# Kernel tuning notes

Hardware: AMD Instinct MI355X
Metric: run time of the kernel (lower is better)

Reference implementation:

```python
import jax, jax.numpy as jnp
import numpy as np

CLASS_NUM = 6
N = 8388608


def setup_inputs() -> dict:
    key = jax.random.key(0)
    k1, k2, k3 = jax.random.split(key, 3)
    inputs = jax.random.normal(k1, (N, CLASS_NUM), dtype=jnp.float32)
    targets = jax.random.randint(k2, (N, 1), 0, CLASS_NUM, dtype=jnp.int32)
    # learned parameter: torch.rand(class_num) -> uniform [0,1)
    class_weight = jax.random.uniform(k3, (CLASS_NUM,), dtype=jnp.float32)
    return {"inputs": inputs, "targets": targets, "class_weight": class_weight}


def reference(inputs, targets, class_weight):
    # weighted argmax over classes: [N]
    preds = jnp.argmax(class_weight * inputs, axis=-1)
    tgt = targets.reshape(-1)  # [N]
    # confusion_matrix[pred, target] += 1  (data-dependent scatter-add histogram)
    cm = jnp.zeros((CLASS_NUM, CLASS_NUM), dtype=jnp.float32)
    cm = cm.at[preds, tgt].add(1.0)
    precision = jnp.diag(cm) / cm.sum(axis=0)
    recall = jnp.diag(cm) / cm.sum(axis=1)
    f1 = 2.0 * precision * recall / (precision + recall)
    loss = -f1.mean()
    return (loss, class_weight)
```

## Files before the change

### kernel.cpp

```cpp
#include <hip/hip_runtime.h>

#define CLS 6

constexpr int HIST_BLOCKS  = 2048;
constexpr int HIST_THREADS = 256;
constexpr int NCOPY        = 4;
constexpr int CM_STRIDE    = 40;

__device__ __forceinline__ int argmax6(float v0, float v1, float v2,
                                       float v3, float v4, float v5) {
    int   pr = 0; float m = v0;
    if (v1 > m) { m = v1; pr = 1; }
    if (v2 > m) { m = v2; pr = 2; }
    if (v3 > m) { m = v3; pr = 3; }
    if (v4 > m) { m = v4; pr = 4; }
    if (v5 > m) { m = v5; pr = 5; }
    return pr;
}

__global__ __launch_bounds__(HIST_THREADS, 8)
void cm_hist_kernel(const float* __restrict__ inputs,
                    const int*   __restrict__ targets,
                    const float* __restrict__ wts,
                    unsigned int* __restrict__ cm,
                    long long n_rows) {
    __shared__ unsigned int cm_s[NCOPY * CM_STRIDE];
    const int tid = threadIdx.x;
    if (tid < NCOPY * CM_STRIDE) cm_s[tid] = 0u;
    __syncthreads();

    const float w0 = wts[0], w1 = wts[1], w2 = wts[2];
    const float w3 = wts[3], w4 = wts[4], w5 = wts[5];

    const float4* __restrict__ in4 = (const float4*)inputs;
    const int4*   __restrict__ tg4 = (const int4*)targets;

    const int copy_base = (tid & (NCOPY - 1)) * CM_STRIDE;

    const long long n_quads = n_rows >> 2;
    const long long stride  = (long long)gridDim.x * blockDim.x;

    for (long long q = (long long)blockIdx.x * blockDim.x + tid;
         q < n_quads; q += stride) {
        const long long b = 6 * q;
        float4 f0 = in4[b + 0];
        float4 f1 = in4[b + 1];
        float4 f2 = in4[b + 2];
        float4 f3 = in4[b + 3];
        float4 f4 = in4[b + 4];
        float4 f5 = in4[b + 5];
        int4   t  = tg4[q];

        int p0 = argmax6(f0.x * w0, f0.y * w1, f0.z * w2, f0.w * w3, f1.x * w4, f1.y * w5);
        int p1 = argmax6(f1.z * w0, f1.w * w1, f2.x * w2, f2.y * w3, f2.z * w4, f2.w * w5);
        int p2 = argmax6(f3.x * w0, f3.y * w1, f3.z * w2, f3.w * w3, f4.x * w4, f4.y * w5);
        int p3 = argmax6(f4.z * w0, f4.w * w1, f5.x * w2, f5.y * w3, f5.z * w4, f5.w * w5);

        atomicAdd(&cm_s[copy_base + p0 * CLS + t.x], 1u);
        atomicAdd(&cm_s[copy_base + p1 * CLS + t.y], 1u);
        atomicAdd(&cm_s[copy_base + p2 * CLS + t.z], 1u);
        atomicAdd(&cm_s[copy_base + p3 * CLS + t.w], 1u);
    }

    if (blockIdx.x == 0 && tid == 0) {
        for (long long r = (n_quads << 2); r < n_rows; ++r) {
            int pr = argmax6(inputs[r * CLS + 0] * w0, inputs[r * CLS + 1] * w1,
                             inputs[r * CLS + 2] * w2, inputs[r * CLS + 3] * w3,
                             inputs[r * CLS + 4] * w4, inputs[r * CLS + 5] * w5);
            atomicAdd(&cm_s[pr * CLS + targets[r]], 1u);
        }
    }

    __syncthreads();
    if (tid < CLS * CLS) {
        unsigned int v = cm_s[tid]
                       + cm_s[CM_STRIDE + tid]
                       + cm_s[2 * CM_STRIDE + tid]
                       + cm_s[3 * CM_STRIDE + tid];
        if (v) atomicAdd(&cm[tid], v);
    }
}

__global__ void macro_score_kernel(const unsigned int* __restrict__ cm,
                                   const float* __restrict__ wts,
                                   float* __restrict__ out) {
    if (threadIdx.x == 0) {
        float c[CLS * CLS];
        #pragma unroll
        for (int i = 0; i < CLS * CLS; ++i) c[i] = (float)cm[i];
        float f1sum = 0.0f;
        #pragma unroll
        for (int i = 0; i < CLS; ++i) {
            float col = 0.0f, row = 0.0f;
            #pragma unroll
            for (int j = 0; j < CLS; ++j) {
                col += c[j * CLS + i];
                row += c[i * CLS + j];
            }
            float d  = c[i * CLS + i];
            float pr = d / col;
            float rc = d / row;
            f1sum += 2.0f * pr * rc / (pr + rc);
        }
        out[0] = -(f1sum / (float)CLS);
    }
    if (threadIdx.x < CLS) out[1 + threadIdx.x] = wts[threadIdx.x];
}

extern "C" void kernel_launch(void* const* d_in, const int* in_sizes, int n_in,
                              void* d_out, int out_size, void* d_ws, size_t ws_size,
                              hipStream_t stream) {
    const float* inputs  = (const float*)d_in[0];
    const int*   targets = (const int*)d_in[1];
    const float* wts     = (const float*)d_in[2];
    float*       out     = (float*)d_out;
    unsigned int* cm     = (unsigned int*)d_ws;

    const long long n_rows = (long long)in_sizes[0] / CLS;

    hipMemsetAsync(cm, 0, CLS * CLS * sizeof(unsigned int), stream);
    cm_hist_kernel<<<HIST_BLOCKS, HIST_THREADS, 0, stream>>>(inputs, targets, wts, cm, n_rows);
    macro_score_kernel<<<1, 64, 0, stream>>>(cm, wts, out);
}
```

Before: 301.9 us.

## Fuse macro-F1 finalization into histogram kernel via last-block ticket

Merges the separate scoring kernel into the histogram kernel: each block bumps a ticket counter after its global atomics, and the last block to finish computes F1 from the confusion matrix and writes the outputs. It also switches input loads to nontemporal loads and doubles the number of per-block shared histogram copies to reduce LDS atomic contention. This removes one kernel launch, at the cost of an extra fence and atomic per block and a correctness dependency on memory ordering.

```diff
diff --git a/kernel.cpp b/kernel.cpp
--- a/kernel.cpp
+++ b/kernel.cpp
@@ -4,8 +4,12 @@
 
 constexpr int HIST_BLOCKS  = 2048;
 constexpr int HIST_THREADS = 256;
-constexpr int NCOPY        = 4;
+constexpr int NCOPY        = 8;
 constexpr int CM_STRIDE    = 40;
+constexpr int CM_WORDS     = CLS * CLS;
+
+typedef float fx4 __attribute__((ext_vector_type(4)));
+typedef int   ix4 __attribute__((ext_vector_type(4)));
 
 __device__ __forceinline__ int argmax6(float v0, float v1, float v2,
                                        float v3, float v4, float v5) {
@@ -19,21 +23,22 @@
 }
 
 __global__ __launch_bounds__(HIST_THREADS, 8)
-void cm_hist_kernel(const float* __restrict__ inputs,
-                    const int*   __restrict__ targets,
-                    const float* __restrict__ wts,
-                    unsigned int* __restrict__ cm,
-                    long long n_rows) {
+void cm_fused_kernel(const float* __restrict__ inputs,
+                     const int*   __restrict__ targets,
+                     const float* __restrict__ wts,
+                     unsigned int* __restrict__ ws,
+                     float* __restrict__ out,
+                     long long n_rows) {
     __shared__ unsigned int cm_s[NCOPY * CM_STRIDE];
     const int tid = threadIdx.x;
-    if (tid < NCOPY * CM_STRIDE) cm_s[tid] = 0u;
+    for (int i = tid; i < NCOPY * CM_STRIDE; i += HIST_THREADS) cm_s[i] = 0u;
     __syncthreads();
 
     const float w0 = wts[0], w1 = wts[1], w2 = wts[2];
     const float w3 = wts[3], w4 = wts[4], w5 = wts[5];
 
-    const float4* __restrict__ in4 = (const float4*)inputs;
-    const int4*   __restrict__ tg4 = (const int4*)targets;
+    const fx4* __restrict__ in4 = (const fx4*)inputs;
+    const ix4* __restrict__ tg4 = (const ix4*)targets;
 
     const int copy_base = (tid & (NCOPY - 1)) * CM_STRIDE;
 
@@ -43,13 +48,13 @@
     for (long long q = (long long)blockIdx.x * blockDim.x + tid;
          q < n_quads; q += stride) {
         const long long b = 6 * q;
-        float4 f0 = in4[b + 0];
-        float4 f1 = in4[b + 1];
-        float4 f2 = in4[b + 2];
-        float4 f3 = in4[b + 3];
-        float4 f4 = in4[b + 4];
-        float4 f5 = in4[b + 5];
-        int4   t  = tg4[q];
+        fx4 f0 = __builtin_nontemporal_load(&in4[b + 0]);
+        fx4 f1 = __builtin_nontemporal_load(&in4[b + 1]);
+        fx4 f2 = __builtin_nontemporal_load(&in4[b + 2]);
+        fx4 f3 = __builtin_nontemporal_load(&in4[b + 3]);
+        fx4 f4 = __builtin_nontemporal_load(&in4[b + 4]);
+        fx4 f5 = __builtin_nontemporal_load(&in4[b + 5]);
+        ix4 t  = __builtin_nontemporal_load(&tg4[q]);
 
         int p0 = argmax6(f0.x * w0, f0.y * w1, f0.z * w2, f0.w * w3, f1.x * w4, f1.y * w5);
         int p1 = argmax6(f1.z * w0, f1.w * w1, f2.x * w2, f2.y * w3, f2.z * w4, f2.w * w5);
@@ -72,39 +77,50 @@
     }
 
     __syncthreads();
-    if (tid < CLS * CLS) {
-        unsigned int v = cm_s[tid]
-                       + cm_s[CM_STRIDE + tid]
-                       + cm_s[2 * CM_STRIDE + tid]
-                       + cm_s[3 * CM_STRIDE + tid];
-        if (v) atomicAdd(&cm[tid], v);
+    if (tid < CM_WORDS) {
+        unsigned int v = 0;
+        #pragma unroll
+        for (int c = 0; c < NCOPY; ++c) v += cm_s[c * CM_STRIDE + tid];
+        if (v) atomicAdd(&ws[tid], v);
     }
-}
+    __syncthreads();
 
-__global__ void macro_score_kernel(const unsigned int* __restrict__ cm,
-                                   const float* __restrict__ wts,
-                                   float* __restrict__ out) {
-    if (threadIdx.x == 0) {
-        float c[CLS * CLS];
-        #pragma unroll
-        for (int i = 0; i < CLS * CLS; ++i) c[i] = (float)cm[i];
-        float f1sum = 0.0f;
-        #pragma unroll
-        for (int i = 0; i < CLS; ++i) {
-            float col = 0.0f, row = 0.0f;
+    __shared__ unsigned int lastFlag;
+    if (tid == 0) {
+        __threadfence();
+        unsigned int old = atomicAdd(&ws[CM_WORDS], 1u);
+        lastFlag = (old == (unsigned int)gridDim.x - 1u) ? 1u : 0u;
+    }
+    __syncthreads();
+
+    if (lastFlag) {
+        __shared__ float cmf[CM_WORDS];
+        if (tid < CM_WORDS) {
+            unsigned int v = __hip_atomic_load(&ws[tid], __ATOMIC_RELAXED,
+                                               __HIP_MEMORY_SCOPE_AGENT);
+            cmf[tid] = (float)v;
+        }
+        __syncthreads();
+        if (tid == 0) {
+            float f1sum = 0.0f;
             #pragma unroll
-            for (int j = 0; j < CLS; ++j) {
-                col += c[j * CLS + i];
-                row += c[i * CLS + j];
+            for (int i = 0; i < CLS; ++i) {
+                float col = 0.0f, row = 0.0f;
+                #pragma unroll
+                for (int j = 0; j < CLS; ++j) {
+                    col += cmf[j * CLS + i];
+                    row += cmf[i * CLS + j];
+                }
+                float d  = cmf[i * CLS + i];
+                float pr = d / col;
+                float rc = d / row;
+                f1sum += 2.0f * pr * rc / (pr + rc);
             }
-            float d  = c[i * CLS + i];
-            float pr = d / col;
-            float rc = d / row;
-            f1sum += 2.0f * pr * rc / (pr + rc);
+            out[0] = -(f1sum / (float)CLS);
+            #pragma unroll
+            for (int i = 0; i < CLS; ++i) out[1 + i] = wts[i];
         }
-        out[0] = -(f1sum / (float)CLS);
     }
-    if (threadIdx.x < CLS) out[1 + threadIdx.x] = wts[threadIdx.x];
 }
 
 extern "C" void kernel_launch(void* const* d_in, const int* in_sizes, int n_in,
@@ -114,11 +130,11 @@
     const int*   targets = (const int*)d_in[1];
     const float* wts     = (const float*)d_in[2];
     float*       out     = (float*)d_out;
-    unsigned int* cm     = (unsigned int*)d_ws;
+    unsigned int* ws     = (unsigned int*)d_ws;
 
     const long long n_rows = (long long)in_sizes[0] / CLS;
 
-    hipMemsetAsync(cm, 0, CLS * CLS * sizeof(unsigned int), stream);
-    cm_hist_kernel<<<HIST_BLOCKS, HIST_THREADS, 0, stream>>>(inputs, targets, wts, cm, n_rows);
-    macro_score_kernel<<<1, 64, 0, stream>>>(cm, wts, out);
+    (void)hipMemsetAsync(ws, 0, (CM_WORDS + 1) * sizeof(unsigned int), stream);
+    cm_fused_kernel<<<HIST_BLOCKS, HIST_THREADS, 0, stream>>>(
+        inputs, targets, wts, ws, out, n_rows);
 }
```

After: 418.1 us. 1.38x slower.
